# Performance work log

Measured on AMD Instinct MI355X. Metric: run time of the kernel, lower is better.

Reference implementation:

```python
import jax, jax.numpy as jnp
import numpy as np

HEAD = 8
K_DIM = 64
ROUNDS = 4
BUCKETS = 32
ACN = 1  # attend_chunk_num
SELF_VAL = -100000.0


def across(x, acn=ACN):
    """Concatenate each chunk with its acn left/right neighbor chunks (wrapping).
    x: (..., n_chunks, chunk_size, feat). Rolls along chunk axis (-3), cats along -2.
    Order matches the torch code: left chunks, self, right chunks."""
    shifts = list(range(acn, 0, -1)) + [0] + list(range(-1, -acn - 1, -1))
    return jnp.concatenate([jnp.roll(x, s, axis=-3) for s in shifts], axis=-2)


def gather_seq(src, idx):
    """src: (b,h,s,f); idx: (b,h,r,s) -> (b,h,r,s,f) (per-round permutation gather)."""
    return jnp.take_along_axis(src[:, :, None, :, :], idx[..., None], axis=-2)


def lsh_forward(x, Wq, bq, Wv, bv, Wo, bo, hash_vec):
    b, s, d = x.shape
    h, k, r = HEAD, K_DIM, ROUNDS
    qk = (x @ Wq + bq).reshape(b, s, h, k).transpose(0, 2, 1, 3)  # (b,h,s,k)
    v = (x @ Wv + bv).reshape(b, s, h, k).transpose(0, 2, 1, 3)   # (b,h,s,k)

    # --- LSH hashing: argmax over [-rot, rot] rotations ---
    rot = jnp.einsum('bhsk,hkvr->bhsvr', qk, hash_vec)
    rot = jnp.concatenate([-rot, rot], axis=-2)
    buckets = jnp.argmax(rot, axis=-2).transpose(0, 1, 3, 2)  # (b,h,r,s)

    ticker = jnp.arange(s)
    buckets = buckets * s + ticker  # stable-sort key: bucket major, position minor
    s_ticker = jnp.argsort(buckets, axis=-1)
    s_buckets = jnp.take_along_axis(buckets, s_ticker, axis=-1)
    undo = jnp.argsort(s_ticker, axis=-1)

    s_qk = gather_seq(qk, s_ticker)  # (b,h,r,s,k)
    s_v = gather_seq(v, s_ticker)
    nrm = jnp.maximum(jnp.linalg.norm(s_qk, axis=-1, keepdims=True), 1e-12)
    s_k = s_qk / nrm  # F.normalize(p=2)

    nb = BUCKETS
    cs = s // nb
    cq = s_qk.reshape(b, h, r, nb, cs, k)
    ck = s_k.reshape(b, h, r, nb, cs, k)
    cv = s_v.reshape(b, h, r, nb, cs, k)
    ct = s_ticker.reshape(b, h, r, nb, cs)

    ak = across(ck)                      # (b,h,r,nb,3cs,k)
    av = across(cv)
    at = across(ct[..., None])[..., 0]   # (b,h,r,nb,3cs)

    dots = jnp.einsum('bhrnik,bhrnjk->bhrnij', cq, ak) * (k ** -0.5)
    NEG = -jnp.finfo(dots.dtype).max

    # self-attention penalty mask
    dots = jnp.where(ct[..., :, None] == at[..., None, :], SELF_VAL, dots)

    # different-bucket mask
    bid = (s_buckets // s).reshape(b, h, r, nb, cs)
    abid = across(bid[..., None])[..., 0]
    dots = jnp.where(bid[..., :, None] != abid[..., None, :], NEG, dots)

    # duplicate count across rounds (same bucket id in any round)
    loc = (buckets // s).transpose(0, 1, 3, 2)     # (b,h,s,r)
    s_loc = gather_seq(loc, s_ticker)              # (b,h,r,s,r)
    cl = s_loc.reshape(b, h, r, nb, cs, r)
    al = across(cl)                                # (b,h,r,nb,3cs,r)
    dup = (cl[..., :, None, :] == al[..., None, :, :]).sum(-1).astype(dots.dtype)
    dup = jax.lax.stop_gradient(dup)
    dots = dots - jnp.log(dup + 1e-9)

    lse = jax.nn.logsumexp(dots, axis=-1, keepdims=True)
    p = jnp.exp(dots - lse)
    vo = jnp.einsum('bhrnij,bhrnjk->bhrnik', p, av).reshape(b, h, r, s, k)
    lse = lse.reshape(b, h, r, s)

    # unsort back to original token order
    vo = jnp.take_along_axis(vo, undo[..., None], axis=-2)
    lse = jnp.take_along_axis(lse, undo, axis=-1)

    # combine rounds with softmax over per-round logsumexp
    w = jnp.exp(lse - jax.nn.logsumexp(lse, axis=2, keepdims=True))
    out = (vo * w[..., None]).sum(axis=2)  # (b,h,s,k)
    out = out.transpose(0, 2, 1, 3).reshape(b, s, h * k)
    return out @ Wo + bo  # dropout is identity in eval


def setup_inputs() -> dict:
    key = jax.random.key(0)
    ks = jax.random.split(key, 8)
    b, s, d = 2, 2048, 512
    sc = 1.0 / np.sqrt(d)  # keep activations numerically tame
    return {
        'x': jax.random.normal(ks[0], (b, s, d), jnp.float32),
        'Wq': jax.random.normal(ks[1], (d, d), jnp.float32) * sc,
        'bq': jax.random.normal(ks[2], (d,), jnp.float32) * 0.01,
        'Wv': jax.random.normal(ks[3], (d, d), jnp.float32) * sc,
        'bv': jax.random.normal(ks[4], (d,), jnp.float32) * 0.01,
        'Wo': jax.random.normal(ks[5], (d, d), jnp.float32) * sc,
        'bo': jax.random.normal(ks[6], (d,), jnp.float32) * 0.01,
        'hash_vec': jax.random.normal(ks[7], (HEAD, K_DIM, BUCKETS // 2, ROUNDS), jnp.float32),
    }


def reference(x, Wq, bq, Wv, bv, Wo, bo, hash_vec):
    return lsh_forward(x, Wq, bq, Wv, bv, Wo, bo, hash_vec)
```

## Files before the change

kernel.cpp:

```cpp
#include <hip/hip_runtime.h>
#include <hip/hip_bf16.h>
#include <math.h>

#define WS_ 192
#define NEGF (-3.402823466e+38f)

typedef __attribute__((ext_vector_type(8))) short short8;
typedef __attribute__((ext_vector_type(4))) float f32x4;
typedef __attribute__((ext_vector_type(4))) unsigned int u32x4;

static __device__ __forceinline__ unsigned int f2bf(float f) {
    unsigned int u = __float_as_uint(f);
    return (u + 0x7FFFu + ((u >> 16) & 1u)) >> 16;
}
static __device__ __forceinline__ unsigned int packsplit(float v) {
    unsigned int h = f2bf(v);
    float hf = __uint_as_float(h << 16);
    unsigned int l = f2bf(v - hf);
    return h | (l << 16);
}
static __device__ __forceinline__ void mkfrag(uint4 a, uint4 b, short8 &h, short8 &l) {
    u32x4 hv, lv;
    hv[0] = __builtin_amdgcn_perm(a.y, a.x, 0x05040100u);
    hv[1] = __builtin_amdgcn_perm(a.w, a.z, 0x05040100u);
    hv[2] = __builtin_amdgcn_perm(b.y, b.x, 0x05040100u);
    hv[3] = __builtin_amdgcn_perm(b.w, b.z, 0x05040100u);
    lv[0] = __builtin_amdgcn_perm(a.y, a.x, 0x07060302u);
    lv[1] = __builtin_amdgcn_perm(a.w, a.z, 0x07060302u);
    lv[2] = __builtin_amdgcn_perm(b.y, b.x, 0x07060302u);
    lv[3] = __builtin_amdgcn_perm(b.w, b.z, 0x07060302u);
    h = __builtin_bit_cast(short8, hv);
    l = __builtin_bit_cast(short8, lv);
}
static __device__ __forceinline__ unsigned int cvtpk(float lo, float hi) {
    unsigned int d;
    asm("v_cvt_pk_bf16_f32 %0, %1, %2" : "=v"(d) : "v"(lo), "v"(hi));
    return d;
}

__global__ __launch_bounds__(256) void pack_kernel(const float* __restrict__ x,
                                                   const float* __restrict__ Wv,
                                                   const float* __restrict__ Wo,
                                                   unsigned int* __restrict__ xpk,
                                                   unsigned int* __restrict__ wvT,
                                                   unsigned int* __restrict__ woT) {
    __shared__ unsigned int T[64][65];
    const int bid = blockIdx.x;
    const int tid = threadIdx.x;
    if (bid < 2048) {
        int idx = (bid * 256 + tid) * 4;
        float4 v = *(const float4*)(x + idx);
        uint4 pk = make_uint4(packsplit(v.x), packsplit(v.y), packsplit(v.z), packsplit(v.w));
        *(uint4*)(xpk + idx) = pk;
        return;
    }
    int wb = bid - 2048;
    const float* Wsrc = (wb < 64) ? Wv : Wo;
    unsigned int* Wdst = (wb < 64) ? wvT : woT;
    int t = wb & 63;
    int k0 = (t >> 3) * 64, n0 = (t & 7) * 64;
#pragma unroll
    for (int pass = 0; pass < 16; ++pass) {
        int i = pass * 4 + (tid >> 6);
        int j = tid & 63;
        T[j][i] = packsplit(Wsrc[(size_t)(k0 + i) * 512 + n0 + j]);
    }
    __syncthreads();
#pragma unroll
    for (int pass = 0; pass < 16; ++pass) {
        int j = pass * 4 + (tid >> 6);
        int i = tid & 63;
        Wdst[(size_t)(n0 + j) * 512 + k0 + i] = T[j][i];
    }
}

__global__ __launch_bounds__(256) void gemm_qk_hash(const float* __restrict__ A,
                                                    const float* __restrict__ W,
                                                    const float* __restrict__ bias,
                                                    const float* __restrict__ hv,
                                                    unsigned int* __restrict__ Cpk,
                                                    float* __restrict__ scaleQ,
                                                    int* __restrict__ loc2) {
    __shared__ float BUF[4352];
    float* As = BUF;
    float* Ws = BUF + 2176;
    const int m0 = blockIdx.x * 64;
    const int n0 = blockIdx.y * 64;
    const int tid = threadIdx.x;
    const int ty = tid >> 4, tx = tid & 15;
    const int ci = tid & 7, ri = tid >> 3;
    const int wk = tid >> 4, wt = tid & 15;
    float acc[4][4] = {};
    for (int k0 = 0; k0 < 512; k0 += 32) {
#pragma unroll
        for (int h2 = 0; h2 < 2; ++h2) {
            int i = ri + h2 * 32;
            float4 a4 = *(const float4*)(A + (size_t)(m0 + i) * 512 + k0 + ci * 4);
            As[(ci * 4 + 0) * 68 + i] = a4.x;
            As[(ci * 4 + 1) * 68 + i] = a4.y;
            As[(ci * 4 + 2) * 68 + i] = a4.z;
            As[(ci * 4 + 3) * 68 + i] = a4.w;
        }
#pragma unroll
        for (int h2 = 0; h2 < 2; ++h2) {
            int kk = wk + h2 * 16;
            float4 w4 = *(const float4*)(W + (size_t)(k0 + kk) * 512 + n0 + wt * 4);
            *(float4*)(&Ws[kk * 68 + wt * 4]) = w4;
        }
        __syncthreads();
#pragma unroll
        for (int kk = 0; kk < 32; ++kk) {
            float4 a4 = *(float4*)(&As[kk * 68 + ty * 4]);
            float4 w4 = *(float4*)(&Ws[kk * 68 + tx * 4]);
            float a[4] = {a4.x, a4.y, a4.z, a4.w};
            float w[4] = {w4.x, w4.y, w4.z, w4.w};
#pragma unroll
            for (int i = 0; i < 4; ++i)
#pragma unroll
                for (int j = 0; j < 4; ++j) acc[i][j] += a[i] * w[j];
        }
        __syncthreads();
    }
    const int hh = n0 >> 6;
#pragma unroll
    for (int i = 0; i < 4; ++i) {
        int m = m0 + ty * 4 + i;
        int b = m >> 11, s = m & 2047;
        float v0 = acc[i][0] + bias[n0 + tx * 4 + 0];
        float v1 = acc[i][1] + bias[n0 + tx * 4 + 1];
        float v2 = acc[i][2] + bias[n0 + tx * 4 + 2];
        float v3 = acc[i][3] + bias[n0 + tx * 4 + 3];
        acc[i][0] = v0; acc[i][1] = v1; acc[i][2] = v2; acc[i][3] = v3;
        size_t base = ((size_t)(((b << 3) + hh) * 2048 + s)) * 64 + tx * 4;
        uint4 pk = make_uint4(packsplit(v0), packsplit(v1), packsplit(v2), packsplit(v3));
        *(uint4*)(Cpk + base) = pk;
        float sq = v0 * v0 + v1 * v1 + v2 * v2 + v3 * v3;
        sq += __shfl_xor(sq, 1, 16); sq += __shfl_xor(sq, 2, 16);
        sq += __shfl_xor(sq, 4, 16); sq += __shfl_xor(sq, 8, 16);
        if (tx == 0)
            scaleQ[(size_t)(((b << 3) + hh) * 2048 + s)] = 0.125f / fmaxf(sqrtf(sq), 1e-12f);
    }
#pragma unroll
    for (int j = 0; j < 4; ++j) {
        int f = tx * 4 + j;
        int xm = (f & 7) << 3;
#pragma unroll
        for (int i = 0; i < 4; ++i)
            BUF[f * 68 + ((ty * 4 + i) ^ xm)] = acc[i][j];
    }
    __syncthreads();
    const float* hvb = hv + (size_t)hh * 4096 + tx * 4;
    float rt[4][4] = {};
#pragma unroll 4
    for (int f = 0; f < 64; ++f) {
        float4 q4 = *(float4*)(&BUF[f * 68 + ((ty * 4) ^ ((f & 7) << 3))]);
        float4 h4 = *(const float4*)(hvb + f * 64);
        float q[4] = {q4.x, q4.y, q4.z, q4.w};
        float hw[4] = {h4.x, h4.y, h4.z, h4.w};
#pragma unroll
        for (int i = 0; i < 4; ++i)
#pragma unroll
            for (int j = 0; j < 4; ++j) rt[i][j] += q[i] * hw[j];
    }
    __syncthreads();
#pragma unroll
    for (int i = 0; i < 4; ++i)
        *(float4*)(&BUF[(ty * 4 + i) * 68 + tx * 4]) =
            make_float4(rt[i][0], rt[i][1], rt[i][2], rt[i][3]);
    __syncthreads();
    {
        const int tok = tid >> 2, rr2 = tid & 3;
        float best = -BUF[tok * 68 + rr2];
        int bj = 0;
        for (int j = 1; j < 16; ++j) {
            float v = BUF[tok * 68 + j * 4 + rr2];
            if (-v > best) { best = -v; bj = j; }
        }
        for (int j = 0; j < 16; ++j) {
            float v = BUF[tok * 68 + j * 4 + rr2];
            if (v > best) { best = v; bj = 16 + j; }
        }
        int m = m0 + tok;
        int b = m >> 11, s = m & 2047;
        loc2[((size_t)(((b << 3) + hh) * 2048 + s)) * 4 + rr2] = bj;
    }
}

__global__ __launch_bounds__(256) void gemm_pk(const unsigned int* __restrict__ Apk,
                                               const unsigned int* __restrict__ BT,
                                               const float* __restrict__ bias,
                                               void* __restrict__ Cout, int mode) {
    __shared__ __align__(16) unsigned int As[64 * 32];
    __shared__ __align__(16) unsigned int Bs[64 * 32];
    const int m0 = blockIdx.x * 64;
    const int n0 = blockIdx.y * 64;
    const int tid = threadIdx.x;
    const int lane = tid & 63, wv = tid >> 6;
    const int lx = lane & 15, hi = lane >> 4;
    f32x4 acc[4] = {{0.f,0.f,0.f,0.f},{0.f,0.f,0.f,0.f},{0.f,0.f,0.f,0.f},{0.f,0.f,0.f,0.f}};
    for (int k0 = 0; k0 < 512; k0 += 32) {
#pragma unroll
        for (int u = 0; u < 2; ++u) {
            int qi = u * 256 + tid;
            int row = qi >> 3, qd = qi & 7;
            uint4 a = *(const uint4*)(Apk + (size_t)(m0 + row) * 512 + k0 + qd * 4);
            *(uint4*)(&As[row * 32 + ((qd ^ (row & 7)) << 2)]) = a;
            uint4 b = *(const uint4*)(BT + (size_t)(n0 + row) * 512 + k0 + qd * 4);
            *(uint4*)(&Bs[row * 32 + ((qd ^ (row & 7)) << 2)]) = b;
        }
        __syncthreads();
        int arow = wv * 16 + lx;
        uint4 a0 = *(uint4*)(&As[arow * 32 + (((2 * hi) ^ (arow & 7)) << 2)]);
        uint4 a1 = *(uint4*)(&As[arow * 32 + (((2 * hi + 1) ^ (arow & 7)) << 2)]);
        short8 Ah, Al; mkfrag(a0, a1, Ah, Al);
#pragma unroll
        for (int j = 0; j < 4; ++j) {
            int brow = j * 16 + lx;
            uint4 b0 = *(uint4*)(&Bs[brow * 32 + (((2 * hi) ^ (brow & 7)) << 2)]);
            uint4 b1 = *(uint4*)(&Bs[brow * 32 + (((2 * hi + 1) ^ (brow & 7)) << 2)]);
            short8 Bh2, Bl2; mkfrag(b0, b1, Bh2, Bl2);
            acc[j] = __builtin_amdgcn_mfma_f32_16x16x32_bf16(Ah, Bh2, acc[j], 0, 0, 0);
            acc[j] = __builtin_amdgcn_mfma_f32_16x16x32_bf16(Ah, Bl2, acc[j], 0, 0, 0);
            acc[j] = __builtin_amdgcn_mfma_f32_16x16x32_bf16(Al, Bh2, acc[j], 0, 0, 0);
        }
        __syncthreads();
    }
#pragma unroll
    for (int j = 0; j < 4; ++j) {
        int nn = n0 + j * 16 + lx;
        float bs = bias[nn];
#pragma unroll
        for (int reg = 0; reg < 4; ++reg) {
            int m = m0 + wv * 16 + hi * 4 + reg;
            float val = acc[j][reg] + bs;
            if (mode == 0) {
                int b = m >> 11, ss = m & 2047;
                int hh = nn >> 6, f = nn & 63;
                ((unsigned short*)Cout)[((size_t)(((b << 3) + hh) * 2048 + ss)) * 64 + f] =
                    (unsigned short)f2bf(val);
            } else {
                ((float*)Cout)[(size_t)m * 512 + nn] = val;
            }
        }
    }
}

__global__ __launch_bounds__(1024) void sort_kernel(const int* __restrict__ loc2,
                                                    int* __restrict__ st) {
    __shared__ int hist[32][32];
    __shared__ int off[32][32];
    __shared__ int base[32];
    const int gid = blockIdx.x;
    const int r = gid & 3, bh = gid >> 2;
    const int tid = threadIdx.x;
    const int lane = tid & 63, wvi = tid >> 6;
    const unsigned long long lower_mask =
        (lane == 0) ? 0ull : ((~0ull) >> (64 - lane));

    int myb[2], myrank[2];
#pragma unroll
    for (int si = 0; si < 2; ++si) {
        int seg = wvi * 2 + si;
        int p = seg * 64 + lane;
        int b = loc2[(size_t)(bh * 2048 + p) * 4 + r];
        myb[si] = b;
        myrank[si] = 0;
#pragma unroll 1
        for (int bkt = 0; bkt < 32; ++bkt) {
            unsigned long long m = __ballot(b == bkt);
            if (b == bkt) myrank[si] = __popcll(m & lower_mask);
            if (lane == bkt) hist[seg][bkt] = __popcll(m);
        }
    }
    __syncthreads();
    if (tid < 32) {
        int running = 0;
#pragma unroll 1
        for (int seg = 0; seg < 32; ++seg) {
            off[seg][tid] = running;
            running += hist[seg][tid];
        }
        base[tid] = running;
    }
    __syncthreads();
    if (tid == 0) {
        int acc = 0;
#pragma unroll 1
        for (int b = 0; b < 32; ++b) { int h = base[b]; base[b] = acc; acc += h; }
    }
    __syncthreads();
#pragma unroll
    for (int si = 0; si < 2; ++si) {
        int seg = wvi * 2 + si;
        int p = seg * 64 + lane;
        int b = myb[si];
        st[(size_t)gid * 2048 + base[b] + off[seg][b] + myrank[si]] = p;
    }
}

#define KQUAD(row, qd) (((row) << 6) + ((((qd) ^ ((row) & 15))) << 2))
#define PBASE 6400

__global__ __launch_bounds__(256, 3) void attn_kernel(const unsigned int* __restrict__ qkpk,
                                                      const unsigned short* __restrict__ vpk,
                                                      const float* __restrict__ scaleQ,
                                                      const int* __restrict__ loc2,
                                                      const int* __restrict__ st,
                                                      float* __restrict__ lseg,
                                                      float* __restrict__ vog) {
    __shared__ __align__(16) unsigned int U[12800];
    __shared__ float scaleK[WS_];
    __shared__ int Tk[WS_];
    __shared__ int Lp[WS_];

    const int gid = blockIdx.x;
    const int n = gid & 31;
    const int r = (gid >> 5) & 3;
    const int bh = gid >> 7;
    const int tid = threadIdx.x;
    const int sbase = (bh * 4 + r) * 2048;
    const int lane = tid & 63;
    const int wv = tid >> 6;
    const int lx = lane & 15;
    const int hi = lane >> 4;

    if (tid < WS_) {
        int w = tid;
        int chunk = (n + 31 + (w >> 6)) & 31;
        int t = st[(size_t)sbase + chunk * 64 + (w & 63)];
        Tk[w] = t;
        int4 l4 = *(const int4*)(loc2 + (size_t)(bh * 2048 + t) * 4);
        Lp[w] = l4.x | (l4.y << 8) | (l4.z << 16) | (l4.w << 24);
        scaleK[w] = scaleQ[bh * 2048 + t];
    }
    __syncthreads();

    const int fs = tid & 15, wsb = tid >> 4;
#pragma unroll
    for (int it = 0; it < 12; ++it) {
        int row = it * 16 + wsb;
        uint4 v4 = *(const uint4*)(qkpk + ((size_t)(bh * 2048 + Tk[row])) * 64 + fs * 4);
        *(uint4*)(&U[KQUAD(row, fs)]) = v4;
    }
    __syncthreads();

    const int qw = 64 + wv * 16 + lx;
    short8 Bh[2], Bl[2];
#pragma unroll
    for (int ks = 0; ks < 2; ++ks) {
        int qd0 = ks * 8 + hi * 2;
        uint4 a = *(const uint4*)(&U[KQUAD(qw, qd0)]);
        uint4 b = *(const uint4*)(&U[KQUAD(qw, qd0 + 1)]);
        mkfrag(a, b, Bh[ks], Bl[ks]);
    }
    f32x4 s[12];
    __builtin_amdgcn_s_setprio(1);
#pragma unroll
    for (int ct = 0; ct < 12; ++ct) {
        f32x4 acc = {0.f, 0.f, 0.f, 0.f};
#pragma unroll
        for (int ks = 0; ks < 2; ++ks) {
            int arow = ct * 16 + lx;
            int qd0 = ks * 8 + hi * 2;
            uint4 a = *(const uint4*)(&U[KQUAD(arow, qd0)]);
            uint4 b = *(const uint4*)(&U[KQUAD(arow, qd0 + 1)]);
            short8 Ah, Al; mkfrag(a, b, Ah, Al);
            acc = __builtin_amdgcn_mfma_f32_16x16x32_bf16(Ah, Bh[ks], acc, 0, 0, 0);
            acc = __builtin_amdgcn_mfma_f32_16x16x32_bf16(Ah, Bl[ks], acc, 0, 0, 0);
            acc = __builtin_amdgcn_mfma_f32_16x16x32_bf16(Al, Bh[ks], acc, 0, 0, 0);
        }
        s[ct] = acc;
    }
    __builtin_amdgcn_s_setprio(0);

    uint4 vl0[3], vl1[3];
#pragma unroll
    for (int it = 0; it < 3; ++it) {
        int idx = it * 256 + tid;
        int pr = idx >> 3, oct = idx & 7;
        vl0[it] = *(const uint4*)(vpk + ((size_t)(bh * 2048 + Tk[pr * 2])) * 64 + oct * 8);
        vl1[it] = *(const uint4*)(vpk + ((size_t)(bh * 2048 + Tk[pr * 2 + 1])) * 64 + oct * 8);
    }
    __syncthreads();

    const int lq = Lp[qw];
    const unsigned int bmask = 0x80u << (r * 8);
    float mx = -3.0e38f;
#pragma unroll
    for (int ct = 0; ct < 12; ++ct) {
#pragma unroll
        for (int rr = 0; rr < 4; ++rr) {
            int c = ct * 16 + hi * 4 + rr;
            float val = s[ct][rr] * scaleK[c];
            unsigned int x = (unsigned int)(lq ^ Lp[c]);
            unsigned int z = ((x & 0x7f7f7f7fu) + 0x7f7f7f7fu) | x;
            unsigned int zm = ~z & 0x80808080u;
            int dup = __popc(zm);
            val = (c == qw) ? -100000.0f : val;
            val = (zm & bmask) ? val : NEGF;
            float ld = (dup < 2) ? 0.0f
                     : (dup == 2) ? 0.69314718f
                     : (dup == 3) ? 1.09861229f : 1.38629436f;
            val -= ld;
            s[ct][rr] = val;
            mx = fmaxf(mx, val);
        }
    }
    mx = fmaxf(mx, __shfl_xor(mx, 16));
    mx = fmaxf(mx, __shfl_xor(mx, 32));
    float ssum = 0.f;
#pragma unroll
    for (int ct = 0; ct < 12; ++ct)
#pragma unroll
        for (int rr = 0; rr < 4; ++rr) {
            float e = __expf(s[ct][rr] - mx);
            s[ct][rr] = e;
            ssum += e;
        }
    ssum += __shfl_xor(ssum, 16);
    ssum += __shfl_xor(ssum, 32);
    float lse = mx + __logf(ssum);
    if (hi == 0) lseg[(size_t)sbase + Tk[qw]] = lse;
    float inv = 1.0f / ssum;

#pragma unroll
    for (int it = 0; it < 3; ++it) {
        int idx = it * 256 + tid;
        int pr = idx >> 3, oct = idx & 7;
        int c0 = pr * 2;
        unsigned int aw[4] = {vl0[it].x, vl0[it].y, vl0[it].z, vl0[it].w};
        unsigned int bw[4] = {vl1[it].x, vl1[it].y, vl1[it].z, vl1[it].w};
#pragma unroll
        for (int j = 0; j < 8; ++j) {
            int f = oct * 8 + j;
            unsigned int w2 = (j & 1)
                ? __builtin_amdgcn_perm(bw[j >> 1], aw[j >> 1], 0x07060302u)
                : __builtin_amdgcn_perm(bw[j >> 1], aw[j >> 1], 0x05040100u);
            int quad = (c0 >> 3) ^ (f & 7) ^ (f >> 3);
            U[f * 100 + (quad << 2) + ((c0 & 7) >> 1)] = w2;
        }
    }
    const int q = wv * 16 + lx;
    const int pxm = (q & 3) << 3;
#pragma unroll
    for (int ct = 0; ct < 12; ++ct) {
        int po = ct * 8 + hi * 2;
        U[PBASE + q * 100 + ((po + 0) ^ pxm)] = cvtpk(s[ct][0] * inv, s[ct][1] * inv);
        U[PBASE + q * 100 + ((po + 1) ^ pxm)] = cvtpk(s[ct][2] * inv, s[ct][3] * inv);
    }
    __syncthreads();

    f32x4 o[4] = {{0.f,0.f,0.f,0.f},{0.f,0.f,0.f,0.f},{0.f,0.f,0.f,0.f},{0.f,0.f,0.f,0.f}};
    const unsigned short* Uh = (const unsigned short*)U;
    __builtin_amdgcn_s_setprio(1);
#pragma unroll
    for (int ks = 0; ks < 6; ++ks) {
        short8 P8 = *(const short8*)(Uh + PBASE * 2 + q * 200 +
                                     (((ks * 16 + hi * 4) ^ pxm) << 1));
#pragma unroll
        for (int ft = 0; ft < 4; ++ft) {
            int f = ft * 16 + lx;
            int quad = (4 * ks + hi) ^ (f & 7) ^ (f >> 3);
            short8 V8 = *(const short8*)(Uh + f * 200 + (quad << 3));
            o[ft] = __builtin_amdgcn_mfma_f32_16x16x32_bf16(V8, P8, o[ft], 0, 0, 0);
        }
    }
    __builtin_amdgcn_s_setprio(0);
    const int tko = Tk[qw];
#pragma unroll
    for (int ft = 0; ft < 4; ++ft) {
        float4 w4 = make_float4(o[ft][0], o[ft][1], o[ft][2], o[ft][3]);
        *(float4*)(vog + ((size_t)sbase + tko) * 64 + ft * 16 + hi * 4) = w4;
    }
}

__global__ __launch_bounds__(256) void combine_kernel(const float* __restrict__ vog,
                                                      const float* __restrict__ lseg,
                                                      unsigned int* __restrict__ attpk) {
    const int gid = blockIdx.x * 256 + threadIdx.x;
    const int kq = gid & 15;
    const int t = (gid >> 4) & 2047;
    const int bh = gid >> 15;
    const int b = bh >> 3, h = bh & 7;
    float l[4];
    float4 vo[4];
#pragma unroll
    for (int r = 0; r < 4; ++r) {
        l[r] = lseg[(size_t)(bh * 4 + r) * 2048 + t];
        vo[r] = *(const float4*)(vog + ((size_t)(bh * 4 + r) * 2048 + t) * 64 + kq * 4);
    }
    float m = fmaxf(fmaxf(l[0], l[1]), fmaxf(l[2], l[3]));
    float ss = expf(l[0] - m) + expf(l[1] - m) + expf(l[2] - m) + expf(l[3] - m);
    float lt = m + logf(ss);
    float o0 = 0.f, o1 = 0.f, o2 = 0.f, o3 = 0.f;
#pragma unroll
    for (int r = 0; r < 4; ++r) {
        float w = expf(l[r] - lt);
        o0 += w * vo[r].x; o1 += w * vo[r].y; o2 += w * vo[r].z; o3 += w * vo[r].w;
    }
    uint4 pk = make_uint4(packsplit(o0), packsplit(o1), packsplit(o2), packsplit(o3));
    *(uint4*)(attpk + ((size_t)(b * 2048 + t)) * 512 + h * 64 + kq * 4) = pk;
}

extern "C" void kernel_launch(void* const* d_in, const int* in_sizes, int n_in,
                              void* d_out, int out_size, void* d_ws, size_t ws_size,
                              hipStream_t stream) {
    const float* x  = (const float*)d_in[0];
    const float* Wq = (const float*)d_in[1];
    const float* bq = (const float*)d_in[2];
    const float* Wv = (const float*)d_in[3];
    const float* bv = (const float*)d_in[4];
    const float* Wo = (const float*)d_in[5];
    const float* bo = (const float*)d_in[6];
    const float* hv = (const float*)d_in[7];

    unsigned int* W = (unsigned int*)d_ws;
    float*          vog    = (float*)W;
    unsigned int*   xpk    = W + 2097152;
    unsigned int*   qkpk   = W + 8388608;
    unsigned short* vpk    = (unsigned short*)(W + 10485760);
    unsigned int*   attpk  = W + 11534336;
    float*          scaleQ = (float*)(W + 13631488);
    int*            loc2   = (int*)(W + 13664256);
    int*            stbuf  = (int*)(W + 13795328);
    float*          lseg   = (float*)(W + 13926400);
    unsigned int*   wvT    = W + 14057472;
    unsigned int*   woT    = W + 14319616;

    dim3 gg(64, 8), blk(256);
    pack_kernel<<<2176, 256, 0, stream>>>(x, Wv, Wo, xpk, wvT, woT);
    gemm_qk_hash<<<gg, blk, 0, stream>>>(x, Wq, bq, hv, qkpk, scaleQ, loc2);
    gemm_pk<<<gg, blk, 0, stream>>>(xpk, wvT, bv, (void*)vpk, 0);
    sort_kernel<<<64, 1024, 0, stream>>>(loc2, stbuf);
    attn_kernel<<<2048, 256, 0, stream>>>(qkpk, vpk, scaleQ, loc2, stbuf, lseg, vog);
    combine_kernel<<<2048, 256, 0, stream>>>(vog, lseg, attpk);
    gemm_pk<<<gg, blk, 0, stream>>>(attpk, woT, bo, d_out, 1);
}
```

Before: 171.0 us.

## Merge pack and QK-hash GEMM into one prep kernel, stream Wq via registers

Fuses the packing/transpose kernel and the QK projection+hash GEMM into a single launch. Blocks 0-511 run the GEMM and the rest do the packing, so the two independent workloads share the GPU concurrently and one kernel launch is saved. The GEMM now stages only the A tile in shared memory and reads Wq rows straight from global memory into registers, which removes the W shared-memory staging but adds more global loads per thread and more register pressure.

```diff
diff --git a/kernel.cpp b/kernel.cpp
--- a/kernel.cpp
+++ b/kernel.cpp
@@ -38,86 +38,91 @@
     return d;
 }
 
-__global__ __launch_bounds__(256) void pack_kernel(const float* __restrict__ x,
+__global__ __launch_bounds__(256) void prep_kernel(const float* __restrict__ A,
+                                                   const float* __restrict__ Wq,
+                                                   const float* __restrict__ bias,
+                                                   const float* __restrict__ hv,
                                                    const float* __restrict__ Wv,
                                                    const float* __restrict__ Wo,
+                                                   unsigned int* __restrict__ Cpk,
+                                                   float* __restrict__ scaleQ,
+                                                   int* __restrict__ loc2,
                                                    unsigned int* __restrict__ xpk,
                                                    unsigned int* __restrict__ wvT,
                                                    unsigned int* __restrict__ woT) {
-    __shared__ unsigned int T[64][65];
+    __shared__ __align__(16) unsigned int SMEM[4352];
     const int bid = blockIdx.x;
     const int tid = threadIdx.x;
-    if (bid < 2048) {
-        int idx = (bid * 256 + tid) * 4;
-        float4 v = *(const float4*)(x + idx);
-        uint4 pk = make_uint4(packsplit(v.x), packsplit(v.y), packsplit(v.z), packsplit(v.w));
-        *(uint4*)(xpk + idx) = pk;
+
+    if (bid >= 512) {
+        int pb = bid - 512;
+        if (pb < 2048) {
+            int idx = (pb * 256 + tid) * 4;
+            float4 v = *(const float4*)(A + idx);
+            uint4 pk = make_uint4(packsplit(v.x), packsplit(v.y),
+                                  packsplit(v.z), packsplit(v.w));
+            *(uint4*)(xpk + idx) = pk;
+            return;
+        }
+        int wb = pb - 2048;
+        const float* Wsrc = (wb < 64) ? Wv : Wo;
+        unsigned int* Wdst = (wb < 64) ? wvT : woT;
+        int t = wb & 63;
+        int k0 = (t >> 3) * 64, n0 = (t & 7) * 64;
+#pragma unroll
+        for (int pass = 0; pass < 16; ++pass) {
+            int i = pass * 4 + (tid >> 6);
+            int j = tid & 63;
+            SMEM[j * 65 + i] = packsplit(Wsrc[(size_t)(k0 + i) * 512 + n0 + j]);
+        }
+        __syncthreads();
+#pragma unroll
+        for (int pass = 0; pass < 16; ++pass) {
+            int j = pass * 4 + (tid >> 6);
+            int i = tid & 63;
+            Wdst[(size_t)(n0 + j) * 512 + k0 + i] = SMEM[j * 65 + i];
+        }
         return;
     }
-    int wb = bid - 2048;
-    const float* Wsrc = (wb < 64) ? Wv : Wo;
-    unsigned int* Wdst = (wb < 64) ? wvT : woT;
-    int t = wb & 63;
-    int k0 = (t >> 3) * 64, n0 = (t & 7) * 64;
-#pragma unroll
-    for (int pass = 0; pass < 16; ++pass) {
-        int i = pass * 4 + (tid >> 6);
-        int j = tid & 63;
-        T[j][i] = packsplit(Wsrc[(size_t)(k0 + i) * 512 + n0 + j]);
-    }
-    __syncthreads();
-#pragma unroll
-    for (int pass = 0; pass < 16; ++pass) {
-        int j = pass * 4 + (tid >> 6);
-        int i = tid & 63;
-        Wdst[(size_t)(n0 + j) * 512 + k0 + i] = T[j][i];
-    }
-}
-
-__global__ __launch_bounds__(256) void gemm_qk_hash(const float* __restrict__ A,
-                                                    const float* __restrict__ W,
-                                                    const float* __restrict__ bias,
-                                                    const float* __restrict__ hv,
-                                                    unsigned int* __restrict__ Cpk,
-                                                    float* __restrict__ scaleQ,
-                                                    int* __restrict__ loc2) {
-    __shared__ float BUF[4352];
-    float* As = BUF;
-    float* Ws = BUF + 2176;
-    const int m0 = blockIdx.x * 64;
-    const int n0 = blockIdx.y * 64;
-    const int tid = threadIdx.x;
+
+    float* BUF = (float*)SMEM;
+    const int m0 = (bid & 63) * 64;
+    const int n0 = (bid >> 6) * 64;
     const int ty = tid >> 4, tx = tid & 15;
     const int ci = tid & 7, ri = tid >> 3;
-    const int wk = tid >> 4, wt = tid & 15;
     float acc[4][4] = {};
     for (int k0 = 0; k0 < 512; k0 += 32) {
-#pragma unroll
-        for (int h2 = 0; h2 < 2; ++h2) {
-            int i = ri + h2 * 32;
-            float4 a4 = *(const float4*)(A + (size_t)(m0 + i) * 512 + k0 + ci * 4);
-            As[(ci * 4 + 0) * 68 + i] = a4.x;
-            As[(ci * 4 + 1) * 68 + i] = a4.y;
-            As[(ci * 4 + 2) * 68 + i] = a4.z;
-            As[(ci * 4 + 3) * 68 + i] = a4.w;
-        }
-#pragma unroll
-        for (int h2 = 0; h2 < 2; ++h2) {
-            int kk = wk + h2 * 16;
-            float4 w4 = *(const float4*)(W + (size_t)(k0 + kk) * 512 + n0 + wt * 4);
-            *(float4*)(&Ws[kk * 68 + wt * 4]) = w4;
+        {
+            float4 a40 = *(const float4*)(A + (size_t)(m0 + ri) * 512 + k0 + ci * 4);
+            float4 a41 = *(const float4*)(A + (size_t)(m0 + ri + 32) * 512 + k0 + ci * 4);
+            BUF[(ci * 4 + 0) * 68 + ri] = a40.x;
+            BUF[(ci * 4 + 1) * 68 + ri] = a40.y;
+            BUF[(ci * 4 + 2) * 68 + ri] = a40.z;
+            BUF[(ci * 4 + 3) * 68 + ri] = a40.w;
+            BUF[(ci * 4 + 0) * 68 + ri + 32] = a41.x;
+            BUF[(ci * 4 + 1) * 68 + ri + 32] = a41.y;
+            BUF[(ci * 4 + 2) * 68 + ri + 32] = a41.z;
+            BUF[(ci * 4 + 3) * 68 + ri + 32] = a41.w;
         }
         __syncthreads();
-#pragma unroll
-        for (int kk = 0; kk < 32; ++kk) {
-            float4 a4 = *(float4*)(&As[kk * 68 + ty * 4]);
-            float4 w4 = *(float4*)(&Ws[kk * 68 + tx * 4]);
-            float a[4] = {a4.x, a4.y, a4.z, a4.w};
-            float w[4] = {w4.x, w4.y, w4.z, w4.w};
-#pragma unroll
-            for (int i = 0; i < 4; ++i)
-#pragma unroll
-                for (int j = 0; j < 4; ++j) acc[i][j] += a[i] * w[j];
+        const float* wp = Wq + (size_t)k0 * 512 + n0 + tx * 4;
+#pragma unroll
+        for (int kq = 0; kq < 4; ++kq) {
+            float4 wr[8];
+#pragma unroll
+            for (int u = 0; u < 8; ++u)
+                wr[u] = *(const float4*)(wp + (size_t)(kq * 8 + u) * 512);
+#pragma unroll
+            for (int u = 0; u < 8; ++u) {
+                int kk = kq * 8 + u;
+                float4 a4 = *(float4*)(&BUF[kk * 68 + ty * 4]);
+                float a[4] = {a4.x, a4.y, a4.z, a4.w};
+                float w[4] = {wr[u].x, wr[u].y, wr[u].z, wr[u].w};
+#pragma unroll
+                for (int i = 0; i < 4; ++i)
+#pragma unroll
+                    for (int j = 0; j < 4; ++j) acc[i][j] += a[i] * w[j];
+            }
         }
         __syncthreads();
     }
@@ -528,8 +533,8 @@
     unsigned int*   woT    = W + 14319616;
 
     dim3 gg(64, 8), blk(256);
-    pack_kernel<<<2176, 256, 0, stream>>>(x, Wv, Wo, xpk, wvT, woT);
-    gemm_qk_hash<<<gg, blk, 0, stream>>>(x, Wq, bq, hv, qkpk, scaleQ, loc2);
+    prep_kernel<<<2688, 256, 0, stream>>>(x, Wq, bq, hv, Wv, Wo,
+                                          qkpk, scaleQ, loc2, xpk, wvT, woT);
     gemm_pk<<<gg, blk, 0, stream>>>(xpk, wvT, bv, (void*)vpk, 0);
     sort_kernel<<<64, 1024, 0, stream>>>(loc2, stbuf);
     attn_kernel<<<2048, 256, 0, stream>>>(qkpk, vpk, scaleQ, loc2, stbuf, lseg, vog);
```

After: 212.3 us. 1.24x slower.
